# Kernel tuning notes

Hardware: AMD Instinct MI355X
Metric: run time of the kernel (lower is better)

The kernel has to match this reference:

```python
import jax, jax.numpy as jnp
import numpy as np

N = 1_000_000
D = 64
HID = 16
G = 8192


def setup_inputs() -> dict:
    key = jax.random.key(0)
    k1, k2, k3, k4, k5, k6 = jax.random.split(key, 6)
    x = jax.random.normal(k1, (N, D), dtype=jnp.float32)
    pos = jax.random.normal(k2, (N, 3), dtype=jnp.float32)
    batch = jnp.sort(jax.random.randint(k3, (N,), 0, G))
    # linear_1: 16 -> 16, linear_2: 16 -> 1 (torch default init scale ~ 1/sqrt(fan_in))
    s1 = 1.0 / np.sqrt(HID)
    w1 = jax.random.uniform(k4, (HID, HID), minval=-s1, maxval=s1, dtype=jnp.float32)
    b1 = jax.random.uniform(k5, (HID,), minval=-s1, maxval=s1, dtype=jnp.float32)
    w2 = jax.random.uniform(k6, (HID, 1), minval=-s1, maxval=s1, dtype=jnp.float32)
    b2 = jnp.zeros((1,), dtype=jnp.float32)
    return {"x": x, "pos": pos, "batch": batch, "num_graphs": G,
            "w1": w1, "b1": b1, "w2": w2, "b2": b2}


def reference(x, pos, batch, num_graphs, w1, b1, w2, b2):
    split = int(x.shape[1] * 0.75)  # take last quarter of features: [N, 16]

    def energy(p, xx):
        s = xx[:, split:]
        s = jax.nn.silu(s @ w1 + b1)          # [N, 16]
        s = s @ w2 + b2                        # [N, 1]
        return jax.ops.segment_sum(s, batch, num_segments=num_graphs)  # [G, 1]

    E_hat = energy(pos, x)
    # F_hat = -dE/dpos. In this standalone module x does not depend on pos,
    # so the gradient is identically zero (faithful to forward as written).
    F_hat = -jax.grad(lambda p: jnp.sum(energy(p, x)))(pos)
    return (E_hat, F_hat)
```

## Files before the change

### kernel.cpp

```cpp
#include <hip/hip_runtime.h>

#define HID 16

__global__ __launch_bounds__(256) void mpainn_energy_kernel(
    const float* __restrict__ x,
    const int* __restrict__ batch,
    const float* __restrict__ w1,
    const float* __restrict__ b1,
    const float* __restrict__ w2,
    const float* __restrict__ b2,
    float* __restrict__ E,
    int n)
{
    __shared__ float w1s[HID * HID];
    __shared__ float b1s[HID];
    __shared__ float w2s[HID];
    __shared__ float b2s;

    const int tid = threadIdx.x;
    if (tid < HID * HID) w1s[tid] = w1[tid];
    if (tid < HID) { b1s[tid] = b1[tid]; w2s[tid] = w2[tid]; }
    if (tid == 0) b2s = b2[0];
    __syncthreads();

    const long long i = (long long)blockIdx.x * blockDim.x + tid;
    const int lane = tid & 63;

    float e = 0.0f;
    int b = -1;
    if (i < n) {
        b = batch[i];

        const float4* p = (const float4*)(x + i * 64 + 48);
        float4 v0 = p[0], v1 = p[1], v2 = p[2], v3 = p[3];
        float s[16] = { v0.x, v0.y, v0.z, v0.w,
                        v1.x, v1.y, v1.z, v1.w,
                        v2.x, v2.y, v2.z, v2.w,
                        v3.x, v3.y, v3.z, v3.w };

        float h[16];
        #pragma unroll
        for (int j = 0; j < 16; ++j) h[j] = b1s[j];

        #pragma unroll
        for (int k = 0; k < 16; ++k) {
            const float sk = s[k];
            #pragma unroll
            for (int j = 0; j < 16; ++j) h[j] += sk * w1s[k * 16 + j];
        }

        e = b2s;
        #pragma unroll
        for (int j = 0; j < 16; ++j) {
            const float a = h[j];
            const float sig = 1.0f / (1.0f + __expf(-a));
            e += (a * sig) * w2s[j];
        }
    }

    #pragma unroll
    for (int d = 1; d < 64; d <<= 1) {
        const float oe = __shfl_up(e, (unsigned)d, 64);
        const int   ob = __shfl_up(b, (unsigned)d, 64);
        if (lane >= d && ob == b) e += oe;
    }
    const int nb = __shfl_down(b, 1, 64);
    const bool last_of_run = (lane == 63) || (nb != b);
    if (i < n && last_of_run) atomicAdd(&E[b], e);
}

extern "C" void kernel_launch(void* const* d_in, const int* in_sizes, int n_in,
                              void* d_out, int out_size, void* d_ws, size_t ws_size,
                              hipStream_t stream)
{
    const float* x     = (const float*)d_in[0];
    const int*   batch = (const int*)d_in[2];
    const float* w1    = (const float*)d_in[4];
    const float* b1    = (const float*)d_in[5];
    const float* w2    = (const float*)d_in[6];
    const float* b2    = (const float*)d_in[7];

    const int n = in_sizes[2];
    float* out = (float*)d_out;

    hipMemsetAsync(d_out, 0, (size_t)out_size * sizeof(float), stream);

    const int block = 256;
    const int grid = (n + block - 1) / block;
    mpainn_energy_kernel<<<grid, block, 0, stream>>>(x, batch, w1, b1, w2, b2, out, n);
}
```

Baseline: 39.17 us.

## Process two nodes per thread and fuse force zeroing into energy kernel

Each thread now evaluates the MLP for two consecutive nodes and pre-combines them before the wavefront segmented scan. This halves the number of shuffle-scan steps and atomics per node. The zeroing of the force output is moved from the memset into the kernel as nontemporal stores, so the memset only clears the energy slots. The boundary handling for the first node of each pair adds extra shuffles and conditional atomics.

```diff
diff --git a/kernel.cpp b/kernel.cpp
--- a/kernel.cpp
+++ b/kernel.cpp
@@ -2,15 +2,17 @@
 
 #define HID 16
 
-__global__ __launch_bounds__(256) void mpainn_energy_kernel(
+typedef float vfloat2 __attribute__((ext_vector_type(2)));
+
+__global__ __launch_bounds__(256) void mpainn_energy2_kernel(
     const float* __restrict__ x,
     const int* __restrict__ batch,
     const float* __restrict__ w1,
     const float* __restrict__ b1,
     const float* __restrict__ w2,
     const float* __restrict__ b2,
-    float* __restrict__ E,
-    int n)
+    float* __restrict__ out,
+    int n, int G)
 {
     __shared__ float w1s[HID * HID];
     __shared__ float b1s[HID];
@@ -23,50 +25,78 @@
     if (tid == 0) b2s = b2[0];
     __syncthreads();
 
-    const long long i = (long long)blockIdx.x * blockDim.x + tid;
+    const long long gid = (long long)blockIdx.x * blockDim.x + tid;
+    const long long i0 = 2 * gid;
+    const long long i1 = i0 + 1;
     const int lane = tid & 63;
 
-    float e = 0.0f;
-    int b = -1;
-    if (i < n) {
-        b = batch[i];
+    float* __restrict__ F = out + G;
+    if (i1 < n) {
+        const vfloat2 z = {0.f, 0.f};
+        vfloat2* fp = (vfloat2*)(F + 6 * gid);
+        __builtin_nontemporal_store(z, fp);
+        __builtin_nontemporal_store(z, fp + 1);
+        __builtin_nontemporal_store(z, fp + 2);
+    } else if (i0 < n) {
+        F[3 * i0] = 0.f; F[3 * i0 + 1] = 0.f; F[3 * i0 + 2] = 0.f;
+    }
 
+    float e0 = 0.f, e1 = 0.f;
+    int b0 = -1, b1k = -1;
+
+    if (i0 < n) b0  = batch[i0];
+    if (i1 < n) b1k = batch[i1];
+
+    auto energy = [&](long long i) -> float {
         const float4* p = (const float4*)(x + i * 64 + 48);
         float4 v0 = p[0], v1 = p[1], v2 = p[2], v3 = p[3];
         float s[16] = { v0.x, v0.y, v0.z, v0.w,
                         v1.x, v1.y, v1.z, v1.w,
                         v2.x, v2.y, v2.z, v2.w,
                         v3.x, v3.y, v3.z, v3.w };
-
         float h[16];
         #pragma unroll
         for (int j = 0; j < 16; ++j) h[j] = b1s[j];
-
         #pragma unroll
         for (int k = 0; k < 16; ++k) {
             const float sk = s[k];
             #pragma unroll
             for (int j = 0; j < 16; ++j) h[j] += sk * w1s[k * 16 + j];
         }
-
-        e = b2s;
+        float e = b2s;
         #pragma unroll
         for (int j = 0; j < 16; ++j) {
             const float a = h[j];
             const float sig = 1.0f / (1.0f + __expf(-a));
             e += (a * sig) * w2s[j];
         }
-    }
+        return e;
+    };
+
+    if (i0 < n) e0 = energy(i0);
+    if (i1 < n) e1 = energy(i1);
+
+    float v = (b0 == b1k) ? (e0 + e1) : e1;
+    const int k = b1k;
 
     #pragma unroll
     for (int d = 1; d < 64; d <<= 1) {
-        const float oe = __shfl_up(e, (unsigned)d, 64);
-        const int   ob = __shfl_up(b, (unsigned)d, 64);
-        if (lane >= d && ob == b) e += oe;
+        const float ov = __shfl_up(v, (unsigned)d, 64);
+        const int   ok = __shfl_up(k, (unsigned)d, 64);
+        if (lane >= d && ok == k) v += ov;
     }
-    const int nb = __shfl_down(b, 1, 64);
-    const bool last_of_run = (lane == 63) || (nb != b);
-    if (i < n && last_of_run) atomicAdd(&E[b], e);
+
+    const float pv = __shfl_up(v, 1, 64);
+    const int   pk = __shfl_up(k, 1, 64);
+    if (b0 >= 0 && b0 != k) {
+        float t = e0;
+        if (lane > 0 && pk == b0) t += pv;
+        atomicAdd(&out[b0], t);
+    }
+
+    const int nb0 = __shfl_down(b0, 1, 64);
+    const bool last = (lane == 63) || (nb0 != k);
+    if (k >= 0 && last) atomicAdd(&out[k], v);
 }
 
 extern "C" void kernel_launch(void* const* d_in, const int* in_sizes, int n_in,
@@ -81,11 +111,13 @@
     const float* b2    = (const float*)d_in[7];
 
     const int n = in_sizes[2];
+    const int G = out_size - 3 * n;
     float* out = (float*)d_out;
 
-    hipMemsetAsync(d_out, 0, (size_t)out_size * sizeof(float), stream);
+    (void)hipMemsetAsync(d_out, 0, (size_t)G * sizeof(float), stream);
 
+    const long long pairs = ((long long)n + 1) / 2;
     const int block = 256;
-    const int grid = (n + block - 1) / block;
-    mpainn_energy_kernel<<<grid, block, 0, stream>>>(x, batch, w1, b1, w2, b2, out, n);
+    const int grid = (int)((pairs + block - 1) / block);
+    mpainn_energy2_kernel<<<grid, block, 0, stream>>>(x, batch, w1, b1, w2, b2, out, n, G);
 }
```

After: 36.64 us (median of 2 runs). 1.07x faster.

## Process four nodes per thread and fuse force zeroing into energy kernel

Applied to the files above, without the earlier changes.

Each thread now handles four consecutive nodes. It loads their batch ids as one int4, reuses each row of w1 read from shared memory across all four nodes, and combines the four energies locally before the wavefront segmented scan. The zeroing of the large force output moves into the kernel as nontemporal vector stores, so the memset only clears the energy part. This is meant to cut shared-memory traffic, scan and atomic overhead, and the cost of a separate full-output memset, at the price of higher register pressure and more complex run-boundary logic.

```diff
diff --git a/kernel.cpp b/kernel.cpp
--- a/kernel.cpp
+++ b/kernel.cpp
@@ -1,16 +1,19 @@
 #include <hip/hip_runtime.h>
 
 #define HID 16
+#define NPT 4
 
-__global__ __launch_bounds__(256) void mpainn_energy_kernel(
+typedef float vfloat4 __attribute__((ext_vector_type(4)));
+
+__global__ __launch_bounds__(256) void mpainn_energy4_kernel(
     const float* __restrict__ x,
     const int* __restrict__ batch,
     const float* __restrict__ w1,
     const float* __restrict__ b1,
     const float* __restrict__ w2,
     const float* __restrict__ b2,
-    float* __restrict__ E,
-    int n)
+    float* __restrict__ out,
+    int n, int G)
 {
     __shared__ float w1s[HID * HID];
     __shared__ float b1s[HID];
@@ -23,50 +26,106 @@
     if (tid == 0) b2s = b2[0];
     __syncthreads();
 
-    const long long i = (long long)blockIdx.x * blockDim.x + tid;
+    const long long gid = (long long)blockIdx.x * blockDim.x + tid;
+    const long long i0 = NPT * gid;
     const int lane = tid & 63;
 
-    float e = 0.0f;
-    int b = -1;
-    if (i < n) {
-        b = batch[i];
-
-        const float4* p = (const float4*)(x + i * 64 + 48);
-        float4 v0 = p[0], v1 = p[1], v2 = p[2], v3 = p[3];
-        float s[16] = { v0.x, v0.y, v0.z, v0.w,
-                        v1.x, v1.y, v1.z, v1.w,
-                        v2.x, v2.y, v2.z, v2.w,
-                        v3.x, v3.y, v3.z, v3.w };
-
-        float h[16];
-        #pragma unroll
-        for (int j = 0; j < 16; ++j) h[j] = b1s[j];
-
-        #pragma unroll
-        for (int k = 0; k < 16; ++k) {
-            const float sk = s[k];
-            #pragma unroll
-            for (int j = 0; j < 16; ++j) h[j] += sk * w1s[k * 16 + j];
-        }
-
-        e = b2s;
-        #pragma unroll
-        for (int j = 0; j < 16; ++j) {
-            const float a = h[j];
-            const float sig = 1.0f / (1.0f + __expf(-a));
-            e += (a * sig) * w2s[j];
+    float* __restrict__ F = out + G;
+    if (i0 + NPT - 1 < n) {
+        const vfloat4 z = {0.f, 0.f, 0.f, 0.f};
+        vfloat4* fp = (vfloat4*)(F + 3 * NPT * gid);
+        __builtin_nontemporal_store(z, fp);
+        __builtin_nontemporal_store(z, fp + 1);
+        __builtin_nontemporal_store(z, fp + 2);
+    } else {
+        for (long long i = i0; i < n; ++i) {
+            F[3 * i] = 0.f; F[3 * i + 1] = 0.f; F[3 * i + 2] = 0.f;
         }
     }
 
+    int bk[NPT];
+    if (i0 + NPT - 1 < n) {
+        const int4 bb = *(const int4*)(batch + i0);
+        bk[0] = bb.x; bk[1] = bb.y; bk[2] = bb.z; bk[3] = bb.w;
+    } else {
+        #pragma unroll
+        for (int t = 0; t < NPT; ++t) bk[t] = (i0 + t < n) ? batch[i0 + t] : -1;
+    }
+
+    float s[NPT][16];
+    #pragma unroll
+    for (int t = 0; t < NPT; ++t) {
+        const long long i = i0 + t;
+        if (i < n) {
+            const float4* p = (const float4*)(x + i * 64 + 48);
+            const float4 v0 = p[0], v1 = p[1], v2 = p[2], v3 = p[3];
+            s[t][0]=v0.x; s[t][1]=v0.y; s[t][2]=v0.z; s[t][3]=v0.w;
+            s[t][4]=v1.x; s[t][5]=v1.y; s[t][6]=v1.z; s[t][7]=v1.w;
+            s[t][8]=v2.x; s[t][9]=v2.y; s[t][10]=v2.z; s[t][11]=v2.w;
+            s[t][12]=v3.x; s[t][13]=v3.y; s[t][14]=v3.z; s[t][15]=v3.w;
+        } else {
+            #pragma unroll
+            for (int j = 0; j < 16; ++j) s[t][j] = 0.f;
+        }
+    }
+
+    float h[NPT][16];
+    #pragma unroll
+    for (int t = 0; t < NPT; ++t)
+        #pragma unroll
+        for (int j = 0; j < 16; ++j) h[t][j] = b1s[j];
+
+    #pragma unroll
+    for (int k = 0; k < 16; ++k) {
+        float wk[16];
+        #pragma unroll
+        for (int j = 0; j < 16; ++j) wk[j] = w1s[k * 16 + j];
+        #pragma unroll
+        for (int t = 0; t < NPT; ++t) {
+            const float sk = s[t][k];
+            #pragma unroll
+            for (int j = 0; j < 16; ++j) h[t][j] += sk * wk[j];
+        }
+    }
+
+    float e[NPT];
+    #pragma unroll
+    for (int t = 0; t < NPT; ++t) {
+        float acc = b2s;
+        #pragma unroll
+        for (int j = 0; j < 16; ++j) {
+            const float a = h[t][j];
+            const float sig = 1.0f / (1.0f + __expf(-a));
+            acc += (a * sig) * w2s[j];
+        }
+        e[t] = acc;
+    }
+
+    const int k3 = bk[NPT - 1];
+    float v = e[3];
+    if (bk[2] == k3) { v += e[2]; if (bk[1] == bk[2]) { v += e[1]; if (bk[0] == bk[1]) v += e[0]; } }
+
     #pragma unroll
     for (int d = 1; d < 64; d <<= 1) {
-        const float oe = __shfl_up(e, (unsigned)d, 64);
-        const int   ob = __shfl_up(b, (unsigned)d, 64);
-        if (lane >= d && ob == b) e += oe;
+        const float ov = __shfl_up(v, (unsigned)d, 64);
+        const int   ok = __shfl_up(k3, (unsigned)d, 64);
+        if (lane >= d && ok == k3) v += ov;
     }
-    const int nb = __shfl_down(b, 1, 64);
-    const bool last_of_run = (lane == 63) || (nb != b);
-    if (i < n && last_of_run) atomicAdd(&E[b], e);
+
+    const float pv = __shfl_up(v, 1, 64);
+    const int   pk = __shfl_up(k3, 1, 64);
+
+    float acc = (lane > 0 && pk == bk[0]) ? pv : 0.f;
+    acc += e[0];
+    if (bk[0] != bk[1]) { if (bk[0] >= 0) atomicAdd(&out[bk[0]], acc); acc = 0.f; }
+    acc += e[1];
+    if (bk[1] != bk[2]) { if (bk[1] >= 0) atomicAdd(&out[bk[1]], acc); acc = 0.f; }
+    acc += e[2];
+    if (bk[2] != k3)    { if (bk[2] >= 0) atomicAdd(&out[bk[2]], acc); }
+
+    const int nb0 = __shfl_down(bk[0], 1, 64);
+    const bool last = (lane == 63) || (nb0 != k3);
+    if (k3 >= 0 && last) atomicAdd(&out[k3], v);
 }
 
 extern "C" void kernel_launch(void* const* d_in, const int* in_sizes, int n_in,
@@ -81,11 +140,13 @@
     const float* b2    = (const float*)d_in[7];
 
     const int n = in_sizes[2];
+    const int G = out_size - 3 * n;
     float* out = (float*)d_out;
 
-    hipMemsetAsync(d_out, 0, (size_t)out_size * sizeof(float), stream);
+    (void)hipMemsetAsync(d_out, 0, (size_t)G * sizeof(float), stream);
 
+    const long long threads = ((long long)n + NPT - 1) / NPT;
     const int block = 256;
-    const int grid = (n + block - 1) / block;
-    mpainn_energy_kernel<<<grid, block, 0, stream>>>(x, batch, w1, b1, w2, b2, out, n);
+    const int grid = (int)((threads + block - 1) / block);
+    mpainn_energy4_kernel<<<grid, block, 0, stream>>>(x, batch, w1, b1, w2, b2, out, n, G);
 }
```

Result: faster. 38.01 us (-3.0%).

## Fuse force zeroing into energy kernel and stage x tail through LDS

Applied to the files above, without the earlier changes.

The kernel now zeroes the force output (3N floats) itself with nontemporal vector stores, and the host memset covers only the G energy entries. That removes the separate memset over the large output buffer. Each row's 16-feature tail is loaded into shared memory with four threads per row before compute, to get more coalesced global reads. The cost is extra LDS traffic, shared memory use that may lower occupancy, and a heavier kernel body.

```diff
diff --git a/kernel.cpp b/kernel.cpp
--- a/kernel.cpp
+++ b/kernel.cpp
@@ -1,54 +1,88 @@
 #include <hip/hip_runtime.h>
 
 #define HID 16
+#define XS_STRIDE 20
 
-__global__ __launch_bounds__(256) void mpainn_energy_kernel(
+typedef float vfloat4 __attribute__((ext_vector_type(4)));
+
+__global__ __launch_bounds__(256) void mpainn_coal_kernel(
     const float* __restrict__ x,
     const int* __restrict__ batch,
     const float* __restrict__ w1,
     const float* __restrict__ b1,
     const float* __restrict__ w2,
     const float* __restrict__ b2,
-    float* __restrict__ E,
-    int n)
+    float* __restrict__ out,
+    int n, int G)
 {
     __shared__ float w1s[HID * HID];
     __shared__ float b1s[HID];
     __shared__ float w2s[HID];
     __shared__ float b2s;
+    __shared__ float xs[256 * XS_STRIDE];
 
     const int tid = threadIdx.x;
-    if (tid < HID * HID) w1s[tid] = w1[tid];
+    w1s[tid] = w1[tid];
     if (tid < HID) { b1s[tid] = b1[tid]; w2s[tid] = w2[tid]; }
     if (tid == 0) b2s = b2[0];
+
+    const long long r0 = (long long)blockIdx.x * 256;
+
+    {
+        const int c  = tid & 3;
+        const int rb = tid >> 2;
+        #pragma unroll
+        for (int g = 0; g < 4; ++g) {
+            const int rl = rb + 64 * g;
+            const long long row = r0 + rl;
+            if (row < n) {
+                const vfloat4 v = *(const vfloat4*)(x + row * 64 + 48 + 4 * c);
+                *(vfloat4*)(xs + rl * XS_STRIDE + 4 * c) = v;
+            }
+        }
+    }
+
+    {
+        float* __restrict__ F = out + G;
+        const long long fstart = 3 * r0;
+        const long long fend   = 3 * (long long)n;
+        const long long fblk_end = fstart + 768;
+        if (fblk_end <= fend) {
+            if (tid < 192) {
+                const vfloat4 z = {0.f, 0.f, 0.f, 0.f};
+                __builtin_nontemporal_store(z, (vfloat4*)(F + fstart + 4 * tid));
+            }
+        } else {
+            for (long long idx = fstart + tid; idx < fend; idx += 256) F[idx] = 0.f;
+        }
+    }
+
+    const long long i = r0 + tid;
+    int b = -1;
+    if (i < n) b = batch[i];
+
     __syncthreads();
 
-    const long long i = (long long)blockIdx.x * blockDim.x + tid;
-    const int lane = tid & 63;
-
-    float e = 0.0f;
-    int b = -1;
+    float e = 0.f;
     if (i < n) {
-        b = batch[i];
-
-        const float4* p = (const float4*)(x + i * 64 + 48);
-        float4 v0 = p[0], v1 = p[1], v2 = p[2], v3 = p[3];
+        const float* xr = xs + tid * XS_STRIDE;
+        const vfloat4 v0 = *(const vfloat4*)(xr + 0);
+        const vfloat4 v1 = *(const vfloat4*)(xr + 4);
+        const vfloat4 v2 = *(const vfloat4*)(xr + 8);
+        const vfloat4 v3 = *(const vfloat4*)(xr + 12);
         float s[16] = { v0.x, v0.y, v0.z, v0.w,
                         v1.x, v1.y, v1.z, v1.w,
                         v2.x, v2.y, v2.z, v2.w,
                         v3.x, v3.y, v3.z, v3.w };
-
         float h[16];
         #pragma unroll
         for (int j = 0; j < 16; ++j) h[j] = b1s[j];
-
         #pragma unroll
         for (int k = 0; k < 16; ++k) {
             const float sk = s[k];
             #pragma unroll
             for (int j = 0; j < 16; ++j) h[j] += sk * w1s[k * 16 + j];
         }
-
         e = b2s;
         #pragma unroll
         for (int j = 0; j < 16; ++j) {
@@ -58,6 +92,7 @@
         }
     }
 
+    const int lane = tid & 63;
     #pragma unroll
     for (int d = 1; d < 64; d <<= 1) {
         const float oe = __shfl_up(e, (unsigned)d, 64);
@@ -66,7 +101,7 @@
     }
     const int nb = __shfl_down(b, 1, 64);
     const bool last_of_run = (lane == 63) || (nb != b);
-    if (i < n && last_of_run) atomicAdd(&E[b], e);
+    if (b >= 0 && last_of_run) atomicAdd(&out[b], e);
 }
 
 extern "C" void kernel_launch(void* const* d_in, const int* in_sizes, int n_in,
@@ -81,11 +116,12 @@
     const float* b2    = (const float*)d_in[7];
 
     const int n = in_sizes[2];
+    const int G = out_size - 3 * n;
     float* out = (float*)d_out;
 
-    hipMemsetAsync(d_out, 0, (size_t)out_size * sizeof(float), stream);
+    (void)hipMemsetAsync(d_out, 0, (size_t)G * sizeof(float), stream);
 
     const int block = 256;
     const int grid = (n + block - 1) / block;
-    mpainn_energy_kernel<<<grid, block, 0, stream>>>(x, batch, w1, b1, w2, b2, out, n);
+    mpainn_coal_kernel<<<grid, block, 0, stream>>>(x, batch, w1, b1, w2, b2, out, n, G);
 }
```

Measured after the change: 38.84 us. Within noise of the previous version (-0.8%).
